# Optimization experiments

Hardware: AMD Instinct MI355X
Metric: run time of the kernel (lower is better)

## Reference

```python
import jax, jax.numpy as jnp
import numpy as np

NEW_SEQ_LEN = 150  # hard-coded in the original forward


def _interp_one(x, length):
    """PyTorch F.interpolate(mode='linear', align_corners=False) on x[:length].
    x: [T, D] float, length: scalar int. Returns [NEW_SEQ_LEN, D]."""
    lf = length.astype(jnp.float32)
    scale = lf / NEW_SEQ_LEN
    src = (jnp.arange(NEW_SEQ_LEN, dtype=jnp.float32) + 0.5) * scale - 0.5
    src = jnp.maximum(src, 0.0)
    i0 = jnp.floor(src).astype(jnp.int32)
    i0 = jnp.minimum(i0, length - 1)
    i1 = jnp.minimum(i0 + 1, length - 1)
    w = (src - i0.astype(jnp.float32))[:, None]  # [150, 1]
    return x[i0] * (1.0 - w) + x[i1] * w


_interp_batch = jax.vmap(_interp_one)  # ragged per-sample interpolation, fused over batch


def setup_inputs() -> dict:
    key = jax.random.key(0)
    ks = jax.random.split(key, 8)
    B, T, C_IMU, C_EMG, EMB, CSD = 2048, 512, 48, 16, 64, 256
    x_imu = jax.random.normal(ks[0], (B, T, C_IMU), jnp.float32)
    x_emg = jax.random.normal(ks[1], (B, T, C_EMG), jnp.float32)
    lens = jax.random.randint(ks[2], (B,), 160, T + 1, jnp.int32)  # >= NEW_SEQ_LEN
    w_emb_imu = jax.random.normal(ks[3], (C_IMU, EMB), jnp.float32) / np.sqrt(C_IMU)
    b_emb_imu = jnp.zeros((EMB,), jnp.float32)
    w_emb_emg = jax.random.normal(ks[4], (C_EMG, EMB), jnp.float32) / np.sqrt(C_EMG)
    b_emb_emg = jnp.zeros((EMB,), jnp.float32)
    w_proj = jax.random.normal(ks[5], (NEW_SEQ_LEN * EMB, CSD), jnp.float32) / np.sqrt(NEW_SEQ_LEN * EMB)
    b_proj = jnp.zeros((CSD,), jnp.float32)
    return {"x_imu": x_imu, "x_emg": x_emg, "lens": lens,
            "w_emb_imu": w_emb_imu, "b_emb_imu": b_emb_imu,
            "w_emb_emg": w_emb_emg, "b_emb_emg": b_emb_emg,
            "w_proj": w_proj, "b_proj": b_proj}


def reference(x_imu, x_emg, lens, w_emb_imu, b_emb_imu, w_emb_emg, b_emb_emg, w_proj, b_proj):
    B = x_imu.shape[0]
    # embedding nets (per-timestep linear encoders) -> [B, T, 64]
    seq_imu = jnp.einsum('btc,ce->bte', x_imu, w_emb_imu) + b_emb_imu
    seq_emg = jnp.einsum('btc,ce->bte', x_emg, w_emb_emg) + b_emb_emg
    # ragged linear interpolation of each sample's first lens[i] steps to 150
    seq_imu = _interp_batch(seq_imu, lens)  # [B, 150, 64]
    seq_emg = _interp_batch(seq_emg, lens)
    # flatten and project; NOTE: original code applies linear_proj_imu to BOTH
    out_imu = seq_imu.reshape(B, -1) @ w_proj + b_proj
    out_emg = seq_emg.reshape(B, -1) @ w_proj + b_proj
    return (out_imu, out_emg)
```

## Files before the change

### kernel.cpp

```cpp
#include <hip/hip_runtime.h>

#define NEWL 150
#define EMBD 64
#define NCOL 256
#define CIMU 48
#define CEMG 16

#define KIMU (NEWL * CIMU)
#define KEMG (NEWL * CEMG)
#define KSTI 225
#define KSTE 75
#define NCI 6
#define NCE 2

typedef __bf16 bf16x8_t __attribute__((ext_vector_type(8)));
typedef __bf16 bf16x4_t __attribute__((ext_vector_type(4)));
typedef float f32x4_t __attribute__((ext_vector_type(4)));

__device__ __forceinline__ f32x4_t mfma16(bf16x8_t a, bf16x8_t b, f32x4_t c) {
  return __builtin_amdgcn_mfma_f32_16x16x32_bf16(a, b, c, 0, 0, 0);
}

template <int C, int KST>
__device__ void wcomb_body(const float* __restrict__ wemb,
                           const float* __restrict__ wreg_src,
                           __bf16* __restrict__ wpk, int s, int j) {
  float wreg[EMBD];
#pragma unroll
  for (int e = 0; e < EMBD; ++e) wreg[e] = wreg_src[(size_t)e * NCOL];
  const int cb = j >> 4, lr = j & 15;
#pragma unroll
  for (int q = 0; q < C / 8; ++q) {
    const int kq = (s * C) / 8 + q;
    const int ks = kq >> 2, h = kq & 3;
    bf16x8_t tv;
#pragma unroll
    for (int u = 0; u < 8; ++u) {
      const float* we = wemb + (q * 8 + u) * EMBD;
      float acc = 0.f;
#pragma unroll
      for (int e = 0; e < EMBD; ++e) acc = fmaf(we[e], wreg[e], acc);
      tv[u] = (__bf16)acc;
    }
    *(bf16x8_t*)(wpk + (((size_t)cb * KST + ks) * 64 + h * 16 + lr) * 8) = tv;
  }
}

__global__ __launch_bounds__(256) void wcomb_kernel(
    const float* __restrict__ w_emb_imu, const float* __restrict__ w_emb_emg,
    const float* __restrict__ b_emb_imu, const float* __restrict__ b_emb_emg,
    const float* __restrict__ w_proj,
    __bf16* __restrict__ wpk_imu, __bf16* __restrict__ wpk_emg,
    float* __restrict__ bpart) {
  const int s = blockIdx.x;
  const int m = blockIdx.y;
  const int j = threadIdx.x;
  const float* wp_base = w_proj + (size_t)s * EMBD * NCOL + j;
  const float* be = (m == 0) ? b_emb_imu : b_emb_emg;
  float bacc = 0.f;
#pragma unroll
  for (int e = 0; e < EMBD; ++e) bacc = fmaf(be[e], wp_base[(size_t)e * NCOL], bacc);
  bpart[((size_t)m * NEWL + s) * NCOL + j] = bacc;
  if (m == 0)
    wcomb_body<CIMU, KSTI>(w_emb_imu, wp_base, wpk_imu, s, j);
  else
    wcomb_body<CEMG, KSTE>(w_emb_emg, wp_base, wpk_emg, s, j);
}

__global__ __launch_bounds__(512, 2) void fused_kernel(
    const float* __restrict__ x_imu, const float* __restrict__ x_emg,
    const int* __restrict__ lens,
    const __bf16* __restrict__ wpk_imu, const __bf16* __restrict__ wpk_emg,
    const float* __restrict__ b_proj, const float* __restrict__ bpart,
    float* __restrict__ p_imu, float* __restrict__ p_emg,
    float* __restrict__ bias, int B, int T) {
  const int bid = blockIdx.x;
  const int span = B >> 5;
  const int nblk = (NCE + NCI) * span;
  if (bid == nblk) {
    const int j = threadIdx.x;
    if (j < NCOL) {
#pragma unroll
      for (int m = 0; m < 2; ++m) {
        float acc = b_proj[j];
        for (int s = 0; s < NEWL; ++s)
          acc += bpart[((size_t)m * NEWL + s) * NCOL + j];
        bias[m * NCOL + j] = acc;
      }
    }
    return;
  }

  __shared__ __bf16 lds[2][2][3][512];

  const int tid = threadIdx.x;
  const int wv = tid >> 6, l = tid & 63;

  const int cs = bid / span;
  const int mt = bid - cs * span;
  const bool is_imu = cs >= NCE;
  const int c = is_imu ? cs - NCE : cs;

  int g0, NG;
  if (is_imu) {
    if (c < 3) { g0 = 13 * c; NG = 13; }
    else       { g0 = 39 + 12 * (c - 3); NG = 12; }
  } else {
    g0 = (c == 0) ? 0 : 13; NG = c ? 12 : 13;
  }
  const int ks0 = 3 * g0;
  const int sb = is_imu ? 2 * g0 : 6 * g0;

  const __bf16* Wp = is_imu ? wpk_imu : wpk_emg;
  const int KST = is_imu ? KSTI : KSTE;
  float* P = is_imu ? (p_imu + (size_t)c * B * NCOL) : (p_emg + (size_t)c * B * NCOL);

  const size_t PS = (size_t)KST * 512;
  const __bf16* bg = Wp + ((size_t)(wv * 2) * KST + ks0) * 512 + l * 8;

  const int q = tid & 3, rowb = (tid >> 2) & 1;
  const int pid = tid >> 3, b4 = pid & 31, sl = pid >> 5;
  const int pid_e = tid >> 1;
  const int ble = pid_e / 6, se = pid_e - ble * 6, rowe = tid & 1;
  const bool act = is_imu || (tid < 384);
  const int b_g = mt * 32 + (is_imu ? b4 : (act ? ble : 0));
  int lenv = 1;
  float scale = 0.f;
  if (act) { lenv = lens[b_g]; scale = (float)lenv * (1.0f / 150.0f); }

  float gr[16];
  float wS;
  bf16x8_t bB[6];
  f32x4_t acc00 = {0.f, 0.f, 0.f, 0.f}, acc01 = acc00, acc10 = acc00, acc11 = acc00;

#define ISSUE_GI(g2) do {                                                       \
    const int s_ = sb + (g2) * 2 + sl;                                          \
    float src_ = fmaxf(((float)s_ + 0.5f) * scale - 0.5f, 0.0f);                \
    int i0_ = min((int)src_, lenv - 1);                                         \
    int i1_ = min(i0_ + 1, lenv - 1);                                           \
    wS = src_ - (float)i0_;                                                     \
    const float* r_ =                                                           \
        x_imu + ((size_t)b_g * T + (rowb ? i1_ : i0_)) * CIMU + q * 4;          \
    _Pragma("unroll")                                                           \
    for (int t = 0; t < 3; ++t) {                                               \
      float4 v_ = *(const float4*)(r_ + t * 16);                                \
      gr[t * 4 + 0] = v_.x; gr[t * 4 + 1] = v_.y;                               \
      gr[t * 4 + 2] = v_.z; gr[t * 4 + 3] = v_.w;                               \
    }                                                                           \
  } while (0)

#define LERP_WI(BUF) do {                                                       \
    const float wg_ = wS, om_ = 1.0f - wg_;                                     \
    _Pragma("unroll")                                                           \
    for (int t = 0; t < 3; ++t) {                                               \
      float p0_ = __shfl_xor(gr[t * 4 + 0], 4);                                 \
      float p1_ = __shfl_xor(gr[t * 4 + 1], 4);                                 \
      float p2_ = __shfl_xor(gr[t * 4 + 2], 4);                                 \
      float p3_ = __shfl_xor(gr[t * 4 + 3], 4);                                 \
      if (rowb == 0) {                                                          \
        bf16x4_t o_;                                                            \
        o_[0] = (__bf16)(gr[t * 4 + 0] * om_ + p0_ * wg_);                      \
        o_[1] = (__bf16)(gr[t * 4 + 1] * om_ + p1_ * wg_);                      \
        o_[2] = (__bf16)(gr[t * 4 + 2] * om_ + p2_ * wg_);                      \
        o_[3] = (__bf16)(gr[t * 4 + 3] * om_ + p3_ * wg_);                      \
        const int kq_ = sl * 6 + t * 2 + (q >> 1);                              \
        *(bf16x4_t*)(&lds[BUF][b4 >> 4][kq_ >> 2]                               \
                         [((kq_ & 3) * 16 + (b4 & 15)) * 8 + (q & 1) * 4]) = o_;\
      }                                                                         \
    }                                                                           \
  } while (0)

#define ISSUE_GE(g2) do { if (act) {                                            \
    const int s_ = sb + (g2) * 6 + se;                                          \
    float src_ = fmaxf(((float)s_ + 0.5f) * scale - 0.5f, 0.0f);                \
    int i0_ = min((int)src_, lenv - 1);                                         \
    int i1_ = min(i0_ + 1, lenv - 1);                                           \
    wS = src_ - (float)i0_;                                                     \
    const float* r_ = x_emg + ((size_t)b_g * T + (rowe ? i1_ : i0_)) * CEMG;    \
    _Pragma("unroll")                                                           \
    for (int t = 0; t < 4; ++t) {                                               \
      float4 v_ = *(const float4*)(r_ + t * 4);                                 \
      gr[t * 4 + 0] = v_.x; gr[t * 4 + 1] = v_.y;                               \
      gr[t * 4 + 2] = v_.z; gr[t * 4 + 3] = v_.w;                               \
    }                                                                           \
  } } while (0)

#define LERP_WE(BUF) do { if (act) {                                            \
    const float wg_ = wS, om_ = 1.0f - wg_;                                     \
    _Pragma("unroll")                                                           \
    for (int t2 = 0; t2 < 2; ++t2) {                                            \
      float pv_[8];                                                             \
      _Pragma("unroll")                                                         \
      for (int u = 0; u < 8; ++u) pv_[u] = __shfl_xor(gr[t2 * 8 + u], 1);       \
      if (rowe == 0) {                                                          \
        bf16x8_t o_;                                                            \
        _Pragma("unroll")                                                       \
        for (int u = 0; u < 8; ++u)                                             \
          o_[u] = (__bf16)(gr[t2 * 8 + u] * om_ + pv_[u] * wg_);                \
        const int kq_ = se * 2 + t2;                                            \
        *(bf16x8_t*)(&lds[BUF][ble >> 4][kq_ >> 2]                              \
                         [((kq_ & 3) * 16 + (ble & 15)) * 8]) = o_;             \
      }                                                                         \
    }                                                                           \
  } } while (0)

#define ISSUE_B(g1) do {                                                        \
    const __bf16* pb_ = bg + (size_t)((g1) * 3) * 512;                          \
    _Pragma("unroll")                                                           \
    for (int ks = 0; ks < 3; ++ks) {                                            \
      bB[ks * 2 + 0] = *(const bf16x8_t*)(pb_ + (size_t)ks * 512);              \
      bB[ks * 2 + 1] = *(const bf16x8_t*)(pb_ + PS + (size_t)ks * 512);         \
    }                                                                           \
  } while (0)

#define COMPUTE(Pp) do {                                                        \
    _Pragma("unroll")                                                           \
    for (int ks = 0; ks < 3; ++ks) {                                            \
      bf16x8_t a0_ = *(const bf16x8_t*)(&lds[Pp][0][ks][l * 8]);                \
      bf16x8_t a1_ = *(const bf16x8_t*)(&lds[Pp][1][ks][l * 8]);                \
      acc00 = mfma16(a0_, bB[ks * 2 + 0], acc00);                               \
      acc01 = mfma16(a0_, bB[ks * 2 + 1], acc01);                               \
      acc10 = mfma16(a1_, bB[ks * 2 + 0], acc10);                               \
      acc11 = mfma16(a1_, bB[ks * 2 + 1], acc11);                               \
    }                                                                           \
  } while (0)

  if (is_imu) { ISSUE_GI(0); LERP_WI(0); }
  else        { ISSUE_GE(0); LERP_WE(0); }
  ISSUE_B(0);
  __syncthreads();

  for (int p = 0; p < NG; ++p) {
    const int more = (p + 1 < NG);
    if (more) { if (is_imu) ISSUE_GI(p + 1); else ISSUE_GE(p + 1); }
    COMPUTE(p & 1);
    if (more) ISSUE_B(p + 1);
    if (more) { if (is_imu) LERP_WI((p + 1) & 1); else LERP_WE((p + 1) & 1); }
    __syncthreads();
  }

  const int lh = l >> 4, lr = l & 15;
  float* Pb = P + (size_t)(mt * 32 + lh * 4) * NCOL + wv * 32 + lr;
#pragma unroll
  for (int jj = 0; jj < 4; ++jj) {
    Pb[(size_t)jj * NCOL] = acc00[jj];
    Pb[(size_t)jj * NCOL + 16] = acc01[jj];
    Pb[(size_t)(16 + jj) * NCOL] = acc10[jj];
    Pb[(size_t)(16 + jj) * NCOL + 16] = acc11[jj];
  }
#undef ISSUE_GI
#undef LERP_WI
#undef ISSUE_GE
#undef LERP_WE
#undef ISSUE_B
#undef COMPUTE
}

__global__ __launch_bounds__(256) void combine_kernel(
    const float* __restrict__ bias, const float* __restrict__ p_imu,
    const float* __restrict__ p_emg, float* __restrict__ out, int B) {
  const int b = blockIdx.x, m = blockIdx.y, j = threadIdx.x;
  const size_t n = (size_t)B * NCOL;
  const size_t o = (size_t)b * NCOL + j;
  if (m == 0) {
    float v = bias[j];
#pragma unroll
    for (int c = 0; c < NCI; ++c) v += p_imu[c * n + o];
    out[o] = v;
  } else {
    float v = bias[NCOL + j];
#pragma unroll
    for (int c = 0; c < NCE; ++c) v += p_emg[c * n + o];
    out[n + o] = v;
  }
}

extern "C" void kernel_launch(void* const* d_in, const int* in_sizes, int n_in,
                              void* d_out, int out_size, void* d_ws, size_t ws_size,
                              hipStream_t stream) {
  const float* x_imu     = (const float*)d_in[0];
  const float* x_emg     = (const float*)d_in[1];
  const int*   lens      = (const int*)d_in[2];
  const float* w_emb_imu = (const float*)d_in[3];
  const float* b_emb_imu = (const float*)d_in[4];
  const float* w_emb_emg = (const float*)d_in[5];
  const float* b_emb_emg = (const float*)d_in[6];
  const float* w_proj    = (const float*)d_in[7];
  const float* b_proj    = (const float*)d_in[8];
  float* out = (float*)d_out;

  const int B = in_sizes[2];
  const int T = in_sizes[0] / (B * CIMU);

  char* ws = (char*)d_ws;
  __bf16* wpk_imu = (__bf16*)ws;  ws += (size_t)NCOL * KIMU * 2;
  __bf16* wpk_emg = (__bf16*)ws;  ws += (size_t)NCOL * KEMG * 2;
  float*  bias    = (float*)ws;   ws += 2 * NCOL * 4;
  float*  bpart   = (float*)ws;   ws += (size_t)2 * NEWL * NCOL * 4;
  float*  p_imu   = (float*)ws;   ws += (size_t)NCI * B * NCOL * 4;
  float*  p_emg   = (float*)ws;   ws += (size_t)NCE * B * NCOL * 4;

  wcomb_kernel<<<dim3(NEWL, 2), 256, 0, stream>>>(
      w_emb_imu, w_emb_emg, b_emb_imu, b_emb_emg, w_proj, wpk_imu, wpk_emg, bpart);
  const int span = B >> 5;
  const int nblk = (NCE + NCI) * span + 1;
  fused_kernel<<<nblk, 512, 0, stream>>>(x_imu, x_emg, lens, wpk_imu, wpk_emg,
                                         b_proj, bpart, p_imu, p_emg, bias, B, T);
  combine_kernel<<<dim3(B, 2), 256, 0, stream>>>(bias, p_imu, p_emg, out, B);
}
```

Before: 82.89 us.

## Widen IMU tiles to 64 rows and split K into 12 chunks

The IMU path now has each block cover 64 batch rows instead of 32, with 4x2 MFMA accumulators per wave, so every B-fragment loaded from the packed weights feeds twice as many MFMAs. To keep enough blocks in flight, the IMU K dimension is split into 12 chunks instead of 6. Each thread also loads both interpolation source rows itself instead of exchanging them through cross-lane shuffles. In exchange, partial-sum traffic to the combine kernel doubles, register use per thread rises, and the block index mapping hard-codes 32 row tiles (mt = u0 & 31), which only holds for B=2048.

```diff
diff --git a/kernel.cpp b/kernel.cpp
--- a/kernel.cpp
+++ b/kernel.cpp
@@ -10,7 +10,7 @@
 #define KEMG (NEWL * CEMG)
 #define KSTI 225
 #define KSTE 75
-#define NCI 6
+#define NCI 12
 #define NCE 2
 
 typedef __bf16 bf16x8_t __attribute__((ext_vector_type(8)));
@@ -75,8 +75,9 @@
     float* __restrict__ p_imu, float* __restrict__ p_emg,
     float* __restrict__ bias, int B, int T) {
   const int bid = blockIdx.x;
-  const int span = B >> 5;
-  const int nblk = (NCE + NCI) * span;
+  const int spanE = B >> 5;
+  const int spanI = B >> 6;
+  const int nblk = NCE * spanE + NCI * spanI;
   if (bid == nblk) {
     const int j = threadIdx.x;
     if (j < NCOL) {
@@ -91,47 +92,38 @@
     return;
   }
 
-  __shared__ __bf16 lds[2][2][3][512];
+  __shared__ __bf16 lds[2][4][3][512];
 
   const int tid = threadIdx.x;
   const int wv = tid >> 6, l = tid & 63;
-
-  const int cs = bid / span;
-  const int mt = bid - cs * span;
-  const bool is_imu = cs >= NCE;
-  const int c = is_imu ? cs - NCE : cs;
-
-  int g0, NG;
+  const bool is_imu = bid >= NCE * spanE;
+
   if (is_imu) {
-    if (c < 3) { g0 = 13 * c; NG = 13; }
-    else       { g0 = 39 + 12 * (c - 3); NG = 12; }
-  } else {
-    g0 = (c == 0) ? 0 : 13; NG = c ? 12 : 13;
-  }
-  const int ks0 = 3 * g0;
-  const int sb = is_imu ? 2 * g0 : 6 * g0;
-
-  const __bf16* Wp = is_imu ? wpk_imu : wpk_emg;
-  const int KST = is_imu ? KSTI : KSTE;
-  float* P = is_imu ? (p_imu + (size_t)c * B * NCOL) : (p_emg + (size_t)c * B * NCOL);
-
-  const size_t PS = (size_t)KST * 512;
-  const __bf16* bg = Wp + ((size_t)(wv * 2) * KST + ks0) * 512 + l * 8;
-
-  const int q = tid & 3, rowb = (tid >> 2) & 1;
-  const int pid = tid >> 3, b4 = pid & 31, sl = pid >> 5;
-  const int pid_e = tid >> 1;
-  const int ble = pid_e / 6, se = pid_e - ble * 6, rowe = tid & 1;
-  const bool act = is_imu || (tid < 384);
-  const int b_g = mt * 32 + (is_imu ? b4 : (act ? ble : 0));
-  int lenv = 1;
-  float scale = 0.f;
-  if (act) { lenv = lens[b_g]; scale = (float)lenv * (1.0f / 150.0f); }
-
-  float gr[16];
-  float wS;
-  bf16x8_t bB[6];
-  f32x4_t acc00 = {0.f, 0.f, 0.f, 0.f}, acc01 = acc00, acc10 = acc00, acc11 = acc00;
+    const int u0 = bid - NCE * spanE;
+    const int c = u0 >> 5, mt = u0 & 31;
+    int g0, NG;
+    if (c < 3) { g0 = 7 * c; NG = 7; }
+    else       { g0 = 21 + 6 * (c - 3); NG = 6; }
+    const int ks0 = 3 * g0;
+    const int sb = 2 * g0;
+    float* P = p_imu + (size_t)c * B * NCOL;
+    const size_t PS = (size_t)KSTI * 512;
+    const __bf16* bg = wpk_imu + ((size_t)(wv * 2) * KSTI + ks0) * 512 + l * 8;
+
+    const int q = tid & 3, sl = (tid >> 2) & 1, b6 = tid >> 3;
+    const int b_g = mt * 64 + b6;
+    const int lenv = lens[b_g];
+    const float scale = (float)lenv * (1.0f / 150.0f);
+    const float* xg = x_imu + (size_t)b_g * T * CIMU + q * 4;
+
+    float gr[24];
+    float wS;
+    bf16x8_t bB[6];
+    f32x4_t acc[4][2];
+#pragma unroll
+    for (int rp = 0; rp < 4; ++rp)
+#pragma unroll
+      for (int cp = 0; cp < 2; ++cp) acc[rp][cp] = (f32x4_t){0.f, 0.f, 0.f, 0.f};
 
 #define ISSUE_GI(g2) do {                                                       \
     const int s_ = sb + (g2) * 2 + sl;                                          \
@@ -139,13 +131,16 @@
     int i0_ = min((int)src_, lenv - 1);                                         \
     int i1_ = min(i0_ + 1, lenv - 1);                                           \
     wS = src_ - (float)i0_;                                                     \
-    const float* r_ =                                                           \
-        x_imu + ((size_t)b_g * T + (rowb ? i1_ : i0_)) * CIMU + q * 4;          \
+    const float* r0_ = xg + (size_t)i0_ * CIMU;                                 \
+    const float* r1_ = xg + (size_t)i1_ * CIMU;                                 \
     _Pragma("unroll")                                                           \
     for (int t = 0; t < 3; ++t) {                                               \
-      float4 v_ = *(const float4*)(r_ + t * 16);                                \
+      float4 v_ = *(const float4*)(r0_ + t * 16);                               \
       gr[t * 4 + 0] = v_.x; gr[t * 4 + 1] = v_.y;                               \
       gr[t * 4 + 2] = v_.z; gr[t * 4 + 3] = v_.w;                               \
+      float4 u_ = *(const float4*)(r1_ + t * 16);                               \
+      gr[12 + t * 4 + 0] = u_.x; gr[12 + t * 4 + 1] = u_.y;                     \
+      gr[12 + t * 4 + 2] = u_.z; gr[12 + t * 4 + 3] = u_.w;                     \
     }                                                                           \
   } while (0)
 
@@ -153,22 +148,88 @@
     const float wg_ = wS, om_ = 1.0f - wg_;                                     \
     _Pragma("unroll")                                                           \
     for (int t = 0; t < 3; ++t) {                                               \
-      float p0_ = __shfl_xor(gr[t * 4 + 0], 4);                                 \
-      float p1_ = __shfl_xor(gr[t * 4 + 1], 4);                                 \
-      float p2_ = __shfl_xor(gr[t * 4 + 2], 4);                                 \
-      float p3_ = __shfl_xor(gr[t * 4 + 3], 4);                                 \
-      if (rowb == 0) {                                                          \
-        bf16x4_t o_;                                                            \
-        o_[0] = (__bf16)(gr[t * 4 + 0] * om_ + p0_ * wg_);                      \
-        o_[1] = (__bf16)(gr[t * 4 + 1] * om_ + p1_ * wg_);                      \
-        o_[2] = (__bf16)(gr[t * 4 + 2] * om_ + p2_ * wg_);                      \
-        o_[3] = (__bf16)(gr[t * 4 + 3] * om_ + p3_ * wg_);                      \
-        const int kq_ = sl * 6 + t * 2 + (q >> 1);                              \
-        *(bf16x4_t*)(&lds[BUF][b4 >> 4][kq_ >> 2]                               \
-                         [((kq_ & 3) * 16 + (b4 & 15)) * 8 + (q & 1) * 4]) = o_;\
-      }                                                                         \
-    }                                                                           \
-  } while (0)
+      bf16x4_t o_;                                                              \
+      _Pragma("unroll")                                                         \
+      for (int u = 0; u < 4; ++u)                                               \
+        o_[u] = (__bf16)(gr[t * 4 + u] * om_ + gr[12 + t * 4 + u] * wg_);       \
+      const int kq_ = sl * 6 + t * 2 + (q >> 1);                                \
+      *(bf16x4_t*)(&lds[BUF][b6 >> 4][kq_ >> 2]                                 \
+                       [((kq_ & 3) * 16 + (b6 & 15)) * 8 + (q & 1) * 4]) = o_;  \
+    }                                                                           \
+  } while (0)
+
+#define ISSUE_B(g1) do {                                                        \
+    const __bf16* pb_ = bg + (size_t)((g1) * 3) * 512;                          \
+    _Pragma("unroll")                                                           \
+    for (int ks = 0; ks < 3; ++ks) {                                            \
+      bB[ks * 2 + 0] = *(const bf16x8_t*)(pb_ + (size_t)ks * 512);              \
+      bB[ks * 2 + 1] = *(const bf16x8_t*)(pb_ + PS + (size_t)ks * 512);         \
+    }                                                                           \
+  } while (0)
+
+#define COMPUTE_I(Pp) do {                                                      \
+    _Pragma("unroll")                                                           \
+    for (int ks = 0; ks < 3; ++ks) {                                            \
+      bf16x8_t a0_ = *(const bf16x8_t*)(&lds[Pp][0][ks][l * 8]);                \
+      bf16x8_t a1_ = *(const bf16x8_t*)(&lds[Pp][1][ks][l * 8]);                \
+      bf16x8_t a2_ = *(const bf16x8_t*)(&lds[Pp][2][ks][l * 8]);                \
+      bf16x8_t a3_ = *(const bf16x8_t*)(&lds[Pp][3][ks][l * 8]);                \
+      acc[0][0] = mfma16(a0_, bB[ks * 2 + 0], acc[0][0]);                       \
+      acc[0][1] = mfma16(a0_, bB[ks * 2 + 1], acc[0][1]);                       \
+      acc[1][0] = mfma16(a1_, bB[ks * 2 + 0], acc[1][0]);                       \
+      acc[1][1] = mfma16(a1_, bB[ks * 2 + 1], acc[1][1]);                       \
+      acc[2][0] = mfma16(a2_, bB[ks * 2 + 0], acc[2][0]);                       \
+      acc[2][1] = mfma16(a2_, bB[ks * 2 + 1], acc[2][1]);                       \
+      acc[3][0] = mfma16(a3_, bB[ks * 2 + 0], acc[3][0]);                       \
+      acc[3][1] = mfma16(a3_, bB[ks * 2 + 1], acc[3][1]);                       \
+    }                                                                           \
+  } while (0)
+
+    ISSUE_GI(0); LERP_WI(0); ISSUE_B(0);
+    __syncthreads();
+    for (int p = 0; p < NG; ++p) {
+      const int more = (p + 1 < NG);
+      if (more) ISSUE_GI(p + 1);
+      COMPUTE_I(p & 1);
+      if (more) ISSUE_B(p + 1);
+      if (more) LERP_WI((p + 1) & 1);
+      __syncthreads();
+    }
+    const int lh = l >> 4, lr = l & 15;
+    float* Pb = P + (size_t)(mt * 64 + lh * 4) * NCOL + wv * 32 + lr;
+#pragma unroll
+    for (int rp = 0; rp < 4; ++rp)
+#pragma unroll
+      for (int cp = 0; cp < 2; ++cp)
+#pragma unroll
+        for (int jj = 0; jj < 4; ++jj)
+          Pb[(size_t)(rp * 16 + jj) * NCOL + cp * 16] = acc[rp][cp][jj];
+#undef ISSUE_GI
+#undef LERP_WI
+#undef ISSUE_B
+#undef COMPUTE_I
+  } else {
+    const int c = bid / spanE, mt = bid - c * spanE;
+    const int g0 = (c == 0) ? 0 : 13;
+    const int NG = c ? 12 : 13;
+    const int ks0 = 3 * g0;
+    const int sb = 6 * g0;
+    float* P = p_emg + (size_t)c * B * NCOL;
+    const size_t PS = (size_t)KSTE * 512;
+    const __bf16* bg = wpk_emg + ((size_t)(wv * 2) * KSTE + ks0) * 512 + l * 8;
+
+    const int pid_e = tid >> 1;
+    const int ble = pid_e / 6, se = pid_e - ble * 6, rowe = tid & 1;
+    const bool act = tid < 384;
+    const int b_g = mt * 32 + (act ? ble : 0);
+    int lenv = 1;
+    float scale = 0.f;
+    if (act) { lenv = lens[b_g]; scale = (float)lenv * (1.0f / 150.0f); }
+
+    float gr[16];
+    float wS;
+    bf16x8_t bB[6];
+    f32x4_t acc00 = {0.f, 0.f, 0.f, 0.f}, acc01 = acc00, acc10 = acc00, acc11 = acc00;
 
 #define ISSUE_GE(g2) do { if (act) {                                            \
     const int s_ = sb + (g2) * 6 + se;                                          \
@@ -204,7 +265,7 @@
     }                                                                           \
   } } while (0)
 
-#define ISSUE_B(g1) do {                                                        \
+#define ISSUE_BE(g1) do {                                                       \
     const __bf16* pb_ = bg + (size_t)((g1) * 3) * 512;                          \
     _Pragma("unroll")                                                           \
     for (int ks = 0; ks < 3; ++ks) {                                            \
@@ -213,7 +274,7 @@
     }                                                                           \
   } while (0)
 
-#define COMPUTE(Pp) do {                                                        \
+#define COMPUTE_E(Pp) do {                                                      \
     _Pragma("unroll")                                                           \
     for (int ks = 0; ks < 3; ++ks) {                                            \
       bf16x8_t a0_ = *(const bf16x8_t*)(&lds[Pp][0][ks][l * 8]);                \
@@ -225,35 +286,30 @@
     }                                                                           \
   } while (0)
 
-  if (is_imu) { ISSUE_GI(0); LERP_WI(0); }
-  else        { ISSUE_GE(0); LERP_WE(0); }
-  ISSUE_B(0);
-  __syncthreads();
-
-  for (int p = 0; p < NG; ++p) {
-    const int more = (p + 1 < NG);
-    if (more) { if (is_imu) ISSUE_GI(p + 1); else ISSUE_GE(p + 1); }
-    COMPUTE(p & 1);
-    if (more) ISSUE_B(p + 1);
-    if (more) { if (is_imu) LERP_WI((p + 1) & 1); else LERP_WE((p + 1) & 1); }
+    ISSUE_GE(0); LERP_WE(0); ISSUE_BE(0);
     __syncthreads();
-  }
-
-  const int lh = l >> 4, lr = l & 15;
-  float* Pb = P + (size_t)(mt * 32 + lh * 4) * NCOL + wv * 32 + lr;
-#pragma unroll
-  for (int jj = 0; jj < 4; ++jj) {
-    Pb[(size_t)jj * NCOL] = acc00[jj];
-    Pb[(size_t)jj * NCOL + 16] = acc01[jj];
-    Pb[(size_t)(16 + jj) * NCOL] = acc10[jj];
-    Pb[(size_t)(16 + jj) * NCOL + 16] = acc11[jj];
-  }
-#undef ISSUE_GI
-#undef LERP_WI
+    for (int p = 0; p < NG; ++p) {
+      const int more = (p + 1 < NG);
+      if (more) ISSUE_GE(p + 1);
+      COMPUTE_E(p & 1);
+      if (more) ISSUE_BE(p + 1);
+      if (more) LERP_WE((p + 1) & 1);
+      __syncthreads();
+    }
+    const int lh = l >> 4, lr = l & 15;
+    float* Pb = P + (size_t)(mt * 32 + lh * 4) * NCOL + wv * 32 + lr;
+#pragma unroll
+    for (int jj = 0; jj < 4; ++jj) {
+      Pb[(size_t)jj * NCOL] = acc00[jj];
+      Pb[(size_t)jj * NCOL + 16] = acc01[jj];
+      Pb[(size_t)(16 + jj) * NCOL] = acc10[jj];
+      Pb[(size_t)(16 + jj) * NCOL + 16] = acc11[jj];
+    }
 #undef ISSUE_GE
 #undef LERP_WE
-#undef ISSUE_B
-#undef COMPUTE
+#undef ISSUE_BE
+#undef COMPUTE_E
+  }
 }
 
 __global__ __launch_bounds__(256) void combine_kernel(
@@ -302,8 +358,7 @@
 
   wcomb_kernel<<<dim3(NEWL, 2), 256, 0, stream>>>(
       w_emb_imu, w_emb_emg, b_emb_imu, b_emb_emg, w_proj, wpk_imu, wpk_emg, bpart);
-  const int span = B >> 5;
-  const int nblk = (NCE + NCI) * span + 1;
+  const int nblk = NCE * (B >> 5) + NCI * (B >> 6) + 1;
   fused_kernel<<<nblk, 512, 0, stream>>>(x_imu, x_emg, lens, wpk_imu, wpk_emg,
                                          b_proj, bpart, p_imu, p_emg, bias, B, T);
   combine_kernel<<<dim3(B, 2), 256, 0, stream>>>(bias, p_imu, p_emg, out, B);
```

New measurement: 84.31 us. Within noise of the previous version (+1.7%).
